# Performance work log

Hardware: AMD Instinct MI355X
Metric: run time of the kernel (lower is better)

Reference implementation:

```python
import jax, jax.numpy as jnp
import numpy as np

DIM_MODEL = 2048
H, DK, DV, L = 16, 128, 128, 2048
LN_EPS = 1e-5


def setup_inputs() -> dict:
    key = jax.random.key(0)
    ks = jax.random.split(key, 8)
    # xavier-ish scale for weights so softmax logits stay sane
    w_scale = (2.0 / (DIM_MODEL + DK)) ** 0.5
    q = jax.random.normal(ks[0], (1, L, DIM_MODEL), dtype=jnp.float32)
    k = jax.random.normal(ks[1], (1, L, DIM_MODEL), dtype=jnp.float32)
    v = jax.random.normal(ks[2], (1, L, DIM_MODEL), dtype=jnp.float32)
    Wq = jax.random.normal(ks[3], (H, DIM_MODEL, DK), dtype=jnp.float32) * w_scale
    Wk = jax.random.normal(ks[4], (H, DIM_MODEL, DK), dtype=jnp.float32) * w_scale
    Wv = jax.random.normal(ks[5], (H, DIM_MODEL, DV), dtype=jnp.float32) * w_scale
    proj_w = jax.random.normal(ks[6], (H * DV, DIM_MODEL), dtype=jnp.float32) * (1.0 / (H * DV) ** 0.5)
    proj_b = jnp.zeros((DIM_MODEL,), dtype=jnp.float32)
    ln_g = jnp.ones((DIM_MODEL,), dtype=jnp.float32)
    ln_b = jnp.zeros((DIM_MODEL,), dtype=jnp.float32)
    return {"q": q, "k": k, "v": v, "Wq": Wq, "Wk": Wk, "Wv": Wv,
            "proj_w": proj_w, "proj_b": proj_b, "ln_g": ln_g, "ln_b": ln_b}


def reference(q, k, v, Wq, Wk, Wv, proj_w, proj_b, ln_g, ln_b):
    # batch must be 1 (enforced by torch.bmm shape rules in the source)
    residual = q  # (1, L, D)
    qs, kv, vv = q[0], k[0], v[0]  # (L, D)
    dim_model = qs.shape[-1]
    temper = jnp.asarray(dim_model, qs.dtype) ** 0.5  # sqrt(dim_model), NOT sqrt(dk)
    qh = jnp.einsum('ld,hdk->hlk', qs, Wq)  # (H, L, dk)
    kh = jnp.einsum('ld,hdk->hlk', kv, Wk)  # (H, L, dk)
    vh = jnp.einsum('ld,hdv->hlv', vv, Wv)  # (H, L, dv)
    scores = jnp.einsum('hqk,hmk->hqm', qh, kh) / temper  # (H, Lq, Lk)
    # faithful quirk: softmax over dim=1 (the QUERY axis)
    attn = jax.nn.softmax(scores, axis=1)
    # attn_dropout / dropout are identity in eval mode
    out = jnp.einsum('hqm,hmv->hqv', attn, vh)  # (H, Lq, dv)
    # cat(split(out, batch=1, dim=0), dim=-1) == move head axis into features
    Lq = out.shape[1]
    out = jnp.transpose(out, (1, 0, 2)).reshape(Lq, -1)  # (Lq, H*dv)
    out = out @ proj_w + proj_b  # (Lq, dim_model)
    y = out[None] + residual  # (1, Lq, D)
    mu = jnp.mean(y, axis=-1, keepdims=True)
    var = jnp.mean((y - mu) ** 2, axis=-1, keepdims=True)
    y = (y - mu) * jax.lax.rsqrt(var + LN_EPS) * ln_g + ln_b
    return (y, attn)
```

## Files before the change

### kernel.cpp

```cpp
#include <hip/hip_runtime.h>
#include <stdint.h>

#define L 2048
#define DMODEL 2048
#define NH 16

typedef __bf16 bf16x8 __attribute__((ext_vector_type(8)));
typedef float f32x4 __attribute__((ext_vector_type(4)));
typedef short s16x4 __attribute__((ext_vector_type(4)));

__device__ __forceinline__ unsigned short f2bf(float f) {
    union { float f; unsigned int i; } w; w.f = f;
    unsigned int u = w.i;
    unsigned int r = u + 0x7fffu + ((u >> 16) & 1u);
    return (unsigned short)(r >> 16);
}

__device__ __forceinline__ void gload_lds16(const unsigned short* g, unsigned short* l) {
    __builtin_amdgcn_global_load_lds(
        (const __attribute__((address_space(1))) void*)g,
        (__attribute__((address_space(3))) void*)l, 16, 0, 0);
}

template<int CMODE, int BM, int BK, int PSM, int SWZ>
__global__ __launch_bounds__(256, 2)
void gemm_bt(const unsigned short* __restrict__ Ag,
             const unsigned short* __restrict__ B,
             void* __restrict__ C,
             int K, int lda, int ldb, int ldc,
             long long sA, long long sB, long long sC, float alpha,
             float* __restrict__ sums)
{
    constexpr int KC8 = BK / 8;
    constexpr int SWM = (KC8 >= 8) ? 7 : (KC8 - 1);
    constexpr int CA  = BM * BK / 2048;
    constexpr int CB  = BK / 16;
    constexpr int MFR = BM / 32;
    constexpr int KG  = BK / 32;

    __shared__ unsigned short As[2][BM * BK];
    __shared__ unsigned short Bs[2][128 * BK];

    int bx, by, bz;
    if constexpr (SWZ == 1) {
        const int xcd = blockIdx.x & 7, rest = blockIdx.x >> 3;
        bx = 0; by = rest & 15; bz = xcd + 8 * (rest >> 4);
    } else if constexpr (SWZ == 2) {
        const int xcd = blockIdx.x & 7, rest = blockIdx.x >> 3;
        const int inner = rest & 255;
        bx = inner & 15; by = inner >> 4; bz = xcd + 8 * (rest >> 8);
    } else if constexpr (SWZ == 3) {
        const int xcd = blockIdx.x & 7, rest = blockIdx.x >> 3;
        bx = xcd + 8 * (rest >> 5); by = rest & 31; bz = 0;
    } else {
        bx = blockIdx.x; by = blockIdx.y; bz = blockIdx.z;
    }

    const int tid  = threadIdx.x;
    const int wave = tid >> 6;
    const int lane = tid & 63;
    const int quad = lane >> 4;
    const int l16  = lane & 15;

    const int tileN = bx * 128;
    const int tileM = by * BM;

    const long long zA = (CMODE == 3) ? (long long)(bz >> 4) : (long long)bz;
    const unsigned short* A16 = Ag + zA * sA;
    B += (long long)bz * sB;

    const int wm = (wave >> 1) * (BM / 2);
    const int wn = (wave & 1) * 64;

    auto stageB = [&](int kk, int buf) {
        #pragma unroll
        for (int j = 0; j < CB; ++j) {
            const int ch = tid + j * 256;
            const int rb = ch / KC8, sl = (ch % KC8) ^ (rb & SWM);
            gload_lds16(B + (long long)(tileN + rb) * ldb + (kk + sl * 8), &Bs[buf][ch * 8]);
        }
    };
    auto stageA = [&](int kk, int buf) {
        #pragma unroll
        for (int j = 0; j < CA; ++j) {
            const int ch = tid + j * 256;
            const int ra = ch / KC8, sl = (ch % KC8) ^ (ra & SWM);
            gload_lds16(A16 + (long long)(tileM + ra) * lda + (kk + sl * 8), &As[buf][ch * 8]);
        }
    };

    f32x4 acc[MFR][4] = {};
    const int nt = K / BK;

    stageA(0, 0);
    stageB(0, 0);
    __syncthreads();

    int cur = 0;
    for (int t = 0; t < nt; ++t) {
        const int nxt = cur ^ 1;
        const int k0n = (t + 1) * BK;
        if (t + 1 < nt) { stageA(k0n, nxt); stageB(k0n, nxt); }

        bf16x8 af[MFR][KG], bfr[4][KG];
        #pragma unroll
        for (int i = 0; i < MFR; ++i) {
            const int rr = wm + i * 16 + l16;
            #pragma unroll
            for (int g = 0; g < KG; ++g)
                af[i][g] = *(const bf16x8*)(&As[cur][rr * BK + ((g * 32 + quad * 8) ^ ((rr & SWM) << 3))]);
        }
        #pragma unroll
        for (int j = 0; j < 4; ++j) {
            const int rr = wn + j * 16 + l16;
            #pragma unroll
            for (int g = 0; g < KG; ++g)
                bfr[j][g] = *(const bf16x8*)(&Bs[cur][rr * BK + ((g * 32 + quad * 8) ^ ((rr & SWM) << 3))]);
        }
        #pragma unroll
        for (int g = 0; g < KG; ++g)
            #pragma unroll
            for (int i = 0; i < MFR; ++i)
                #pragma unroll
                for (int j = 0; j < 4; ++j)
                    acc[i][j] = __builtin_amdgcn_mfma_f32_16x16x32_bf16(af[i][g], bfr[j][g], acc[i][j], 0, 0, 0);

        __syncthreads();
        cur = nxt;
    }

    const long long cb = (long long)bz * sC;
    const float aEff = (CMODE == 3) ? (bz < 16 ? alpha : 1.0f) : alpha;
    if constexpr (CMODE != 4) {
        #pragma unroll
        for (int i = 0; i < MFR; ++i) {
            const int r0 = tileM + wm + i * 16 + quad * 4;
            #pragma unroll
            for (int j = 0; j < 4; ++j) {
                const int c = tileN + wn + j * 16 + l16;
                f32x4 d = acc[i][j];
                if (CMODE == 0) {
                    unsigned short* Cp = (unsigned short*)C + cb;
                    #pragma unroll
                    for (int r = 0; r < 4; ++r)
                        Cp[(long long)(r0 + r) * ldc + c] = f2bf(d[r] * aEff);
                } else if (CMODE == 1) {
                    unsigned short* Cp = (unsigned short*)C + cb + (long long)c * ldc + r0;
                    s16x4 pk;
                    #pragma unroll
                    for (int r = 0; r < 4; ++r) pk[r] = (short)f2bf(d[r] * aEff);
                    *(s16x4*)Cp = pk;
                } else if (CMODE == 2) {
                    float* Cp = (float*)C + cb;
                    #pragma unroll
                    for (int r = 0; r < 4; ++r)
                        Cp[(long long)(r0 + r) * ldc + c] = d[r] * aEff;
                } else {
                    if (bz < 32) {
                        unsigned short* Cp = (unsigned short*)C + cb;
                        #pragma unroll
                        for (int r = 0; r < 4; ++r)
                            Cp[(long long)(r0 + r) * 128 + c] = f2bf(d[r] * aEff);
                    } else {
                        unsigned short* Cp = (unsigned short*)C + cb + (long long)c * 2048 + r0;
                        s16x4 pk;
                        #pragma unroll
                        for (int r = 0; r < 4; ++r) pk[r] = (short)f2bf(d[r]);
                        *(s16x4*)Cp = pk;
                    }
                }
            }
        }
    }

    if constexpr (PSM) {
        float* sc = sums + (long long)bz * 2048;
        #pragma unroll
        for (int j = 0; j < 4; ++j) {
            float ej = 0.f;
            #pragma unroll
            for (int i = 0; i < MFR; ++i)
                #pragma unroll
                for (int r = 0; r < 4; ++r) ej += __expf(acc[i][j][r]);
            ej += __shfl_xor(ej, 16, 64);
            ej += __shfl_xor(ej, 32, 64);
            if (quad == 0)
                atomicAdd(&sc[tileN + wn + j * 16 + l16], ej);
        }
    }
}

__global__ __launch_bounds__(256, 2)
void fused_pv(const unsigned short* __restrict__ qh,
              const unsigned short* __restrict__ kh,
              const unsigned short* __restrict__ vhT,
              const float* __restrict__ sums,
              float* __restrict__ attn, unsigned short* __restrict__ O)
{
    __shared__ unsigned short qh_s[64 * 128];
    __shared__ unsigned short kh_s[2][32 * 128];
    __shared__ unsigned short vh_s[3][128 * 32];
    __shared__ unsigned short p16[2][64 * 32];

    const int tid = threadIdx.x;
    const int wave = tid >> 6, lane = tid & 63, quad = lane >> 4, l16 = lane & 15;
    const int slot = blockIdx.x >> 3;
    const int qt = slot & 31;
    const int h  = (blockIdx.x & 7) + 8 * (slot >> 5);
    const int wA = wave >> 1, wB = wave & 1;
    const unsigned short* qg = qh + (long long)h * 262144 + (long long)qt * 64 * 128;
    const unsigned short* kg = kh + (long long)h * 262144;
    const unsigned short* vg = vhT + (long long)h * 262144;
    const float* smp = sums + h * 2048;
    float* ap = attn + (long long)h * L * L + (long long)qt * 64 * 2048;

    auto stage_kv = [&](int kt, int kb_, int vb_) {
        #pragma unroll
        for (int jj = 0; jj < 2; ++jj) {
            const int c = tid + jj * 256;
            const int rl = c >> 4, sl = (c & 15) ^ (rl & 7);
            gload_lds16(kg + (long long)(kt * 32 + rl) * 128 + sl * 8, &kh_s[kb_][c * 8]);
        }
        #pragma unroll
        for (int jj = 0; jj < 2; ++jj) {
            const int c = tid + jj * 256;
            const int vd = c >> 2, sl = (c & 3) ^ (vd & 3);
            gload_lds16(vg + (long long)vd * 2048 + kt * 32 + sl * 8, &vh_s[vb_][c * 8]);
        }
    };

    #pragma unroll
    for (int jj = 0; jj < 4; ++jj) {
        const int c = tid + jj * 256;
        const int rl = c >> 4, sl = (c & 15) ^ (rl & 7);
        gload_lds16(qg + (long long)rl * 128 + sl * 8, &qh_s[c * 8]);
    }
    stage_kv(0, 0, 0);
    __syncthreads();

    f32x4 acc_o[2][4] = {};
    const int krow = wA * 16 + l16;

    for (int t = 0; t < 64; ++t) {
        const int cb = t & 1;
        const int vb3 = t % 3;
        if (t < 63) stage_kv(t + 1, cb ^ 1, (t + 1) % 3);

        const int kb = t * 32 + wA * 16 + quad * 4;
        const f32x4 sg4 = *(const f32x4*)(smp + kb);

        bf16x8 af[4];
        #pragma unroll
        for (int g = 0; g < 4; ++g)
            af[g] = *(const bf16x8*)(&kh_s[cb][krow * 128 + ((g * 32 + quad * 8) ^ ((krow & 7) << 3))]);
        f32x4 acc_s[2];
        __builtin_amdgcn_s_setprio(1);
        #pragma unroll
        for (int j = 0; j < 2; ++j) {
            const int q = wB * 32 + j * 16 + l16;
            f32x4 s = {};
            #pragma unroll
            for (int g = 0; g < 4; ++g) {
                bf16x8 bq = *(const bf16x8*)(&qh_s[q * 128 + ((g * 32 + quad * 8) ^ ((q & 7) << 3))]);
                s = __builtin_amdgcn_mfma_f32_16x16x32_bf16(af[g], bq, s, 0, 0, 0);
            }
            acc_s[j] = s;
        }
        __builtin_amdgcn_s_setprio(0);

        f32x4 il4;
        #pragma unroll
        for (int r = 0; r < 4; ++r) il4[r] = __builtin_amdgcn_rcpf(sg4[r]);
        #pragma unroll
        for (int j = 0; j < 2; ++j) {
            const int q = wB * 32 + j * 16 + l16;
            f32x4 p;
            #pragma unroll
            for (int r = 0; r < 4; ++r)
                p[r] = __expf(acc_s[j][r]) * il4[r];
            __builtin_nontemporal_store(p, (f32x4*)(ap + (long long)q * 2048 + kb));
            s16x4 pk;
            #pragma unroll
            for (int r = 0; r < 4; ++r) pk[r] = (short)f2bf(p[r]);
            *(s16x4*)(&p16[cb][q * 32 + ((wA * 16 + quad * 4) ^ ((q & 3) << 3))]) = pk;
        }

        __syncthreads();

        bf16x8 pa[2], vb[4];
        #pragma unroll
        for (int i = 0; i < 2; ++i) {
            const int qq = wA * 32 + i * 16 + l16;
            pa[i] = *(const bf16x8*)(&p16[cb][qq * 32 + ((quad * 8) ^ ((qq & 3) << 3))]);
        }
        #pragma unroll
        for (int j = 0; j < 4; ++j) {
            const int vd = wB * 64 + j * 16 + l16;
            vb[j] = *(const bf16x8*)(&vh_s[vb3][vd * 32 + ((quad * 8) ^ ((vd & 3) << 3))]);
        }
        __builtin_amdgcn_s_setprio(1);
        #pragma unroll
        for (int i = 0; i < 2; ++i)
            #pragma unroll
            for (int j = 0; j < 4; ++j)
                acc_o[i][j] = __builtin_amdgcn_mfma_f32_16x16x32_bf16(pa[i], vb[j], acc_o[i][j], 0, 0, 0);
        __builtin_amdgcn_s_setprio(0);
    }

    #pragma unroll
    for (int i = 0; i < 2; ++i) {
        const int q = qt * 64 + wA * 32 + i * 16 + quad * 4;
        #pragma unroll
        for (int j = 0; j < 4; ++j) {
            const int vd = h * 128 + wB * 64 + j * 16 + l16;
            #pragma unroll
            for (int r = 0; r < 4; ++r)
                O[(long long)(q + r) * 2048 + vd] = f2bf(acc_o[i][j][r]);
        }
    }
}

__global__ __launch_bounds__(256)
void cvt_f2b3(const float* __restrict__ a, const float* __restrict__ b,
              const float* __restrict__ c, unsigned short* __restrict__ out)
{
    const float* in = blockIdx.z == 0 ? a : blockIdx.z == 1 ? b : c;
    const long long i = ((long long)blockIdx.x * 256 + threadIdx.x) * 8;
    const float4 f0 = *(const float4*)(in + i);
    const float4 f1 = *(const float4*)(in + i + 4);
    union { int4 v; unsigned short u[8]; } t;
    t.u[0] = f2bf(f0.x); t.u[1] = f2bf(f0.y); t.u[2] = f2bf(f0.z); t.u[3] = f2bf(f0.w);
    t.u[4] = f2bf(f1.x); t.u[5] = f2bf(f1.y); t.u[6] = f2bf(f1.z); t.u[7] = f2bf(f1.w);
    *(int4*)(out + (long long)blockIdx.z * 4194304 + i) = t.v;
}

__global__ __launch_bounds__(256)
void transpose_f2b(const float* __restrict__ in, unsigned short* __restrict__ out,
                   int rows, int cols)
{
    __shared__ float t[32][33];
    const long long base = (long long)blockIdx.z * rows * cols;
    const int c0 = blockIdx.x * 32, r0 = blockIdx.y * 32;
    const int tx = threadIdx.x, ty0 = threadIdx.y;
    #pragma unroll
    for (int jj = 0; jj < 4; ++jj) {
        const int j = ty0 + jj * 8;
        t[j][tx] = in[base + (long long)(r0 + j) * cols + (c0 + tx)];
    }
    __syncthreads();
    #pragma unroll
    for (int jj = 0; jj < 4; ++jj) {
        const int j = ty0 + jj * 8;
        out[base + (long long)(c0 + j) * rows + (r0 + tx)] = f2bf(t[tx][j]);
    }
}

__global__ __launch_bounds__(256)
void transpose_f2b3(const float* __restrict__ Wq, const float* __restrict__ Wk,
                    const float* __restrict__ Wv, unsigned short* __restrict__ out)
{
    __shared__ float t[32][33];
    const int z = blockIdx.z, widx = z >> 4, h = z & 15;
    const float* in = (widx == 0 ? Wq : widx == 1 ? Wk : Wv) + (long long)h * 2048 * 128;
    unsigned short* o = out + (long long)z * 262144;
    const int c0 = blockIdx.x * 32, r0 = blockIdx.y * 32;
    const int tx = threadIdx.x, ty0 = threadIdx.y;
    #pragma unroll
    for (int jj = 0; jj < 4; ++jj) {
        const int j = ty0 + jj * 8;
        t[j][tx] = in[(long long)(r0 + j) * 128 + (c0 + tx)];
    }
    __syncthreads();
    #pragma unroll
    for (int jj = 0; jj < 4; ++jj) {
        const int j = ty0 + jj * 8;
        o[(long long)(c0 + j) * 2048 + (r0 + tx)] = f2bf(t[tx][j]);
    }
}

__global__ __launch_bounds__(256)
void ln_resid(const float* __restrict__ ypre, const float* __restrict__ resid,
              const float* __restrict__ pb, const float* __restrict__ g,
              const float* __restrict__ bta, float* __restrict__ y)
{
    __shared__ float as_[4], as2_[4];
    const int l = blockIdx.x;
    const int tid = threadIdx.x;
    float v[8]; float s = 0.f, s2 = 0.f;
    #pragma unroll
    for (int i = 0; i < 8; ++i) {
        const int d = tid + i * 256;
        float t = ypre[(long long)l * DMODEL + d] + pb[d] + resid[(long long)l * DMODEL + d];
        v[i] = t; s += t; s2 += t * t;
    }
    #pragma unroll
    for (int off = 32; off > 0; off >>= 1) {
        s  += __shfl_down(s, off, 64);
        s2 += __shfl_down(s2, off, 64);
    }
    const int wave = tid >> 6, lane = tid & 63;
    if (lane == 0) { as_[wave] = s; as2_[wave] = s2; }
    __syncthreads();
    const float S  = as_[0] + as_[1] + as_[2] + as_[3];
    const float S2 = as2_[0] + as2_[1] + as2_[2] + as2_[3];
    const float mu  = S * (1.0f / DMODEL);
    const float var = S2 * (1.0f / DMODEL) - mu * mu;
    const float rs  = rsqrtf(var + 1e-5f);
    #pragma unroll
    for (int i = 0; i < 8; ++i) {
        const int d = tid + i * 256;
        y[(long long)l * DMODEL + d] = (v[i] - mu) * rs * g[d] + bta[d];
    }
}

extern "C" void kernel_launch(void* const* d_in, const int* in_sizes, int n_in,
                              void* d_out, int out_size, void* d_ws, size_t ws_size,
                              hipStream_t stream)
{
    const float* q  = (const float*)d_in[0];
    const float* k  = (const float*)d_in[1];
    const float* v  = (const float*)d_in[2];
    const float* Wq = (const float*)d_in[3];
    const float* Wk = (const float*)d_in[4];
    const float* Wv = (const float*)d_in[5];
    const float* Pw = (const float*)d_in[6];
    const float* Pb = (const float*)d_in[7];
    const float* Lg = (const float*)d_in[8];
    const float* Lb = (const float*)d_in[9];

    float* y    = (float*)d_out;
    float* attn = y + (size_t)L * DMODEL;

    const size_t SEG = (size_t)4194304;
    unsigned short* T0  = (unsigned short*)d_ws;
    unsigned short* qh  = T0 + SEG;
    unsigned short* kh  = qh + SEG;
    unsigned short* vhT = kh + SEG;
    unsigned short* O   = vhT + SEG;
    float* ypre  = (float*)qh;
    float* sums  = (float*)d_ws;

    unsigned short* qkvb = (unsigned short*)attn;
    unsigned short* WT   = qkvb + 3 * SEG;

    const float inv_temper = 0.022097086912079608f;
    dim3 tb(32, 8);

    cvt_f2b3<<<dim3(2048, 1, 3), 256, 0, stream>>>(q, k, v, qkvb);
    transpose_f2b3<<<dim3(4, 64, 48), tb, 0, stream>>>(Wq, Wk, Wv, WT);
    hipMemsetAsync(sums, 0, (size_t)NH * 2048 * sizeof(float), stream);

    gemm_bt<3, 128, 64, 0, 1><<<dim3(768), 256, 0, stream>>>(qkvb, WT, qh,
        2048, 2048, 2048, 0, 4194304LL, 262144LL, 262144LL, inv_temper, nullptr);

    gemm_bt<4, 128, 64, 1, 2><<<dim3(4096), 256, 0, stream>>>(qh, kh, nullptr,
        128, 128, 128, 0, 262144LL, 262144LL, 0LL, 1.0f, sums);

    fused_pv<<<dim3(512), 256, 0, stream>>>(qh, kh, vhT, sums, attn, O);

    transpose_f2b<<<dim3(64, 64, 1), tb, 0, stream>>>(Pw, T0, 2048, 2048);
    gemm_bt<2, 64, 64, 0, 3><<<dim3(512), 256, 0, stream>>>(O, T0, (void*)ypre,
        2048, 2048, 2048, 2048, 0LL, 0LL, 0LL, 1.0f, nullptr);

    ln_resid<<<dim3(2048), 256, 0, stream>>>(ypre, q, Pb, Lg, Lb, y);
}
```

Baseline: 577.2 us.

## Merge prep kernels, add dedicated QK stats kernel, keep Q fragments in registers

Three launches (activation bf16 conversion, weight transpose, memset of the softmax sums) become one prep kernel that dispatches on block index. The QK column-sum pass moves from the generic double-buffered gemm to a dedicated kernel that loads the full K=128 tiles into LDS once and writes no output. fused_pv now keeps each wave's Q fragments in registers loaded straight from global memory instead of staging Q through LDS, which frees LDS. This is meant to cut launch overhead and LDS traffic, at the cost of more register pressure and a larger LDS footprint in stats_qk.

```diff
diff --git a/kernel.cpp b/kernel.cpp
--- a/kernel.cpp
+++ b/kernel.cpp
@@ -22,14 +22,13 @@
         (__attribute__((address_space(3))) void*)l, 16, 0, 0);
 }
 
-template<int CMODE, int BM, int BK, int PSM, int SWZ>
+template<int CMODE, int BM, int BK, int SWZ>
 __global__ __launch_bounds__(256, 2)
 void gemm_bt(const unsigned short* __restrict__ Ag,
              const unsigned short* __restrict__ B,
              void* __restrict__ C,
              int K, int lda, int ldb, int ldc,
-             long long sA, long long sB, long long sC, float alpha,
-             float* __restrict__ sums)
+             long long sA, long long sB, long long sC, float alpha)
 {
     constexpr int KC8 = BK / 8;
     constexpr int SWM = (KC8 >= 8) ? 7 : (KC8 - 1);
@@ -45,10 +44,6 @@
     if constexpr (SWZ == 1) {
         const int xcd = blockIdx.x & 7, rest = blockIdx.x >> 3;
         bx = 0; by = rest & 15; bz = xcd + 8 * (rest >> 4);
-    } else if constexpr (SWZ == 2) {
-        const int xcd = blockIdx.x & 7, rest = blockIdx.x >> 3;
-        const int inner = rest & 255;
-        bx = inner & 15; by = inner >> 4; bz = xcd + 8 * (rest >> 8);
     } else if constexpr (SWZ == 3) {
         const int xcd = blockIdx.x & 7, rest = blockIdx.x >> 3;
         bx = xcd + 8 * (rest >> 5); by = rest & 31; bz = 0;
@@ -131,62 +126,110 @@
 
     const long long cb = (long long)bz * sC;
     const float aEff = (CMODE == 3) ? (bz < 16 ? alpha : 1.0f) : alpha;
-    if constexpr (CMODE != 4) {
-        #pragma unroll
-        for (int i = 0; i < MFR; ++i) {
-            const int r0 = tileM + wm + i * 16 + quad * 4;
-            #pragma unroll
-            for (int j = 0; j < 4; ++j) {
-                const int c = tileN + wn + j * 16 + l16;
-                f32x4 d = acc[i][j];
-                if (CMODE == 0) {
+    #pragma unroll
+    for (int i = 0; i < MFR; ++i) {
+        const int r0 = tileM + wm + i * 16 + quad * 4;
+        #pragma unroll
+        for (int j = 0; j < 4; ++j) {
+            const int c = tileN + wn + j * 16 + l16;
+            f32x4 d = acc[i][j];
+            if (CMODE == 0) {
+                unsigned short* Cp = (unsigned short*)C + cb;
+                #pragma unroll
+                for (int r = 0; r < 4; ++r)
+                    Cp[(long long)(r0 + r) * ldc + c] = f2bf(d[r] * aEff);
+            } else if (CMODE == 1) {
+                unsigned short* Cp = (unsigned short*)C + cb + (long long)c * ldc + r0;
+                s16x4 pk;
+                #pragma unroll
+                for (int r = 0; r < 4; ++r) pk[r] = (short)f2bf(d[r] * aEff);
+                *(s16x4*)Cp = pk;
+            } else if (CMODE == 2) {
+                float* Cp = (float*)C + cb;
+                #pragma unroll
+                for (int r = 0; r < 4; ++r)
+                    Cp[(long long)(r0 + r) * ldc + c] = d[r] * aEff;
+            } else {
+                if (bz < 32) {
                     unsigned short* Cp = (unsigned short*)C + cb;
                     #pragma unroll
                     for (int r = 0; r < 4; ++r)
-                        Cp[(long long)(r0 + r) * ldc + c] = f2bf(d[r] * aEff);
-                } else if (CMODE == 1) {
-                    unsigned short* Cp = (unsigned short*)C + cb + (long long)c * ldc + r0;
+                        Cp[(long long)(r0 + r) * 128 + c] = f2bf(d[r] * aEff);
+                } else {
+                    unsigned short* Cp = (unsigned short*)C + cb + (long long)c * 2048 + r0;
                     s16x4 pk;
                     #pragma unroll
-                    for (int r = 0; r < 4; ++r) pk[r] = (short)f2bf(d[r] * aEff);
+                    for (int r = 0; r < 4; ++r) pk[r] = (short)f2bf(d[r]);
                     *(s16x4*)Cp = pk;
-                } else if (CMODE == 2) {
-                    float* Cp = (float*)C + cb;
-                    #pragma unroll
-                    for (int r = 0; r < 4; ++r)
-                        Cp[(long long)(r0 + r) * ldc + c] = d[r] * aEff;
-                } else {
-                    if (bz < 32) {
-                        unsigned short* Cp = (unsigned short*)C + cb;
-                        #pragma unroll
-                        for (int r = 0; r < 4; ++r)
-                            Cp[(long long)(r0 + r) * 128 + c] = f2bf(d[r] * aEff);
-                    } else {
-                        unsigned short* Cp = (unsigned short*)C + cb + (long long)c * 2048 + r0;
-                        s16x4 pk;
-                        #pragma unroll
-                        for (int r = 0; r < 4; ++r) pk[r] = (short)f2bf(d[r]);
-                        *(s16x4*)Cp = pk;
-                    }
                 }
             }
         }
     }
-
-    if constexpr (PSM) {
-        float* sc = sums + (long long)bz * 2048;
+}
+
+__global__ __launch_bounds__(256, 2)
+void stats_qk(const unsigned short* __restrict__ qh,
+              const unsigned short* __restrict__ kh,
+              float* __restrict__ sums)
+{
+    __shared__ unsigned short As[128 * 128];
+    __shared__ unsigned short Bs[128 * 128];
+
+    const int xcd = blockIdx.x & 7, rest = blockIdx.x >> 3;
+    const int inner = rest & 255;
+    const int bx = inner & 15, by = inner >> 4;
+    const int bz = xcd + 8 * (rest >> 8);
+
+    const int tid = threadIdx.x;
+    const int wave = tid >> 6, lane = tid & 63, quad = lane >> 4, l16 = lane & 15;
+    const int tileN = bx * 128, tileM = by * 128;
+    const int wm = (wave >> 1) * 64, wn = (wave & 1) * 64;
+
+    const unsigned short* A16 = qh + (long long)bz * 262144;
+    const unsigned short* B16 = kh + (long long)bz * 262144;
+
+    #pragma unroll
+    for (int j = 0; j < 8; ++j) {
+        const int ch = tid + j * 256;
+        const int rr = ch >> 4, sl = (ch & 15) ^ (rr & 7);
+        gload_lds16(A16 + (long long)(tileM + rr) * 128 + sl * 8, &As[ch * 8]);
+        gload_lds16(B16 + (long long)(tileN + rr) * 128 + sl * 8, &Bs[ch * 8]);
+    }
+    __syncthreads();
+
+    f32x4 acc[4][4] = {};
+    #pragma unroll
+    for (int g = 0; g < 4; ++g) {
+        bf16x8 af[4], bfr[4];
+        #pragma unroll
+        for (int i = 0; i < 4; ++i) {
+            const int rr = wm + i * 16 + l16;
+            af[i] = *(const bf16x8*)(&As[rr * 128 + ((g * 32 + quad * 8) ^ ((rr & 7) << 3))]);
+        }
         #pragma unroll
         for (int j = 0; j < 4; ++j) {
-            float ej = 0.f;
-            #pragma unroll
-            for (int i = 0; i < MFR; ++i)
-                #pragma unroll
-                for (int r = 0; r < 4; ++r) ej += __expf(acc[i][j][r]);
-            ej += __shfl_xor(ej, 16, 64);
-            ej += __shfl_xor(ej, 32, 64);
-            if (quad == 0)
-                atomicAdd(&sc[tileN + wn + j * 16 + l16], ej);
-        }
+            const int rr = wn + j * 16 + l16;
+            bfr[j] = *(const bf16x8*)(&Bs[rr * 128 + ((g * 32 + quad * 8) ^ ((rr & 7) << 3))]);
+        }
+        #pragma unroll
+        for (int i = 0; i < 4; ++i)
+            #pragma unroll
+            for (int j = 0; j < 4; ++j)
+                acc[i][j] = __builtin_amdgcn_mfma_f32_16x16x32_bf16(af[i], bfr[j], acc[i][j], 0, 0, 0);
+    }
+
+    float* sc = sums + (long long)bz * 2048;
+    #pragma unroll
+    for (int j = 0; j < 4; ++j) {
+        float ej = 0.f;
+        #pragma unroll
+        for (int i = 0; i < 4; ++i)
+            #pragma unroll
+            for (int r = 0; r < 4; ++r) ej += __expf(acc[i][j][r]);
+        ej += __shfl_xor(ej, 16, 64);
+        ej += __shfl_xor(ej, 32, 64);
+        if (quad == 0)
+            atomicAdd(&sc[tileN + wn + j * 16 + l16], ej);
     }
 }
 
@@ -197,7 +240,6 @@
               const float* __restrict__ sums,
               float* __restrict__ attn, unsigned short* __restrict__ O)
 {
-    __shared__ unsigned short qh_s[64 * 128];
     __shared__ unsigned short kh_s[2][32 * 128];
     __shared__ unsigned short vh_s[3][128 * 32];
     __shared__ unsigned short p16[2][64 * 32];
@@ -229,11 +271,13 @@
         }
     };
 
-    #pragma unroll
-    for (int jj = 0; jj < 4; ++jj) {
-        const int c = tid + jj * 256;
-        const int rl = c >> 4, sl = (c & 15) ^ (rl & 7);
-        gload_lds16(qg + (long long)rl * 128 + sl * 8, &qh_s[c * 8]);
+    bf16x8 bq[2][4];
+    #pragma unroll
+    for (int j = 0; j < 2; ++j) {
+        const int q = wB * 32 + j * 16 + l16;
+        #pragma unroll
+        for (int g = 0; g < 4; ++g)
+            bq[j][g] = *(const bf16x8*)(qg + (long long)q * 128 + g * 32 + quad * 8);
     }
     stage_kv(0, 0, 0);
     __syncthreads();
@@ -257,13 +301,10 @@
         __builtin_amdgcn_s_setprio(1);
         #pragma unroll
         for (int j = 0; j < 2; ++j) {
-            const int q = wB * 32 + j * 16 + l16;
             f32x4 s = {};
             #pragma unroll
-            for (int g = 0; g < 4; ++g) {
-                bf16x8 bq = *(const bf16x8*)(&qh_s[q * 128 + ((g * 32 + quad * 8) ^ ((q & 7) << 3))]);
-                s = __builtin_amdgcn_mfma_f32_16x16x32_bf16(af[g], bq, s, 0, 0, 0);
-            }
+            for (int g = 0; g < 4; ++g)
+                s = __builtin_amdgcn_mfma_f32_16x16x32_bf16(af[g], bq[j][g], s, 0, 0, 0);
             acc_s[j] = s;
         }
         __builtin_amdgcn_s_setprio(0);
@@ -321,17 +362,52 @@
 }
 
 __global__ __launch_bounds__(256)
-void cvt_f2b3(const float* __restrict__ a, const float* __restrict__ b,
-              const float* __restrict__ c, unsigned short* __restrict__ out)
-{
-    const float* in = blockIdx.z == 0 ? a : blockIdx.z == 1 ? b : c;
-    const long long i = ((long long)blockIdx.x * 256 + threadIdx.x) * 8;
-    const float4 f0 = *(const float4*)(in + i);
-    const float4 f1 = *(const float4*)(in + i + 4);
-    union { int4 v; unsigned short u[8]; } t;
-    t.u[0] = f2bf(f0.x); t.u[1] = f2bf(f0.y); t.u[2] = f2bf(f0.z); t.u[3] = f2bf(f0.w);
-    t.u[4] = f2bf(f1.x); t.u[5] = f2bf(f1.y); t.u[6] = f2bf(f1.z); t.u[7] = f2bf(f1.w);
-    *(int4*)(out + (long long)blockIdx.z * 4194304 + i) = t.v;
+void prep(const float* __restrict__ q, const float* __restrict__ k,
+          const float* __restrict__ v,
+          const float* __restrict__ Wq, const float* __restrict__ Wk,
+          const float* __restrict__ Wv,
+          unsigned short* __restrict__ qkvb, unsigned short* __restrict__ WT,
+          float* __restrict__ sums)
+{
+    __shared__ float t[32][33];
+    const int bid = blockIdx.x;
+    const int tid = threadIdx.x;
+
+    if (bid < 6144) {
+        const int z = bid >> 11, xb = bid & 2047;
+        const float* in = z == 0 ? q : z == 1 ? k : v;
+        const long long i = ((long long)xb * 256 + tid) * 8;
+        const float4 f0 = *(const float4*)(in + i);
+        const float4 f1 = *(const float4*)(in + i + 4);
+        union { int4 v4; unsigned short u[8]; } tt;
+        tt.u[0] = f2bf(f0.x); tt.u[1] = f2bf(f0.y); tt.u[2] = f2bf(f0.z); tt.u[3] = f2bf(f0.w);
+        tt.u[4] = f2bf(f1.x); tt.u[5] = f2bf(f1.y); tt.u[6] = f2bf(f1.z); tt.u[7] = f2bf(f1.w);
+        *(int4*)(qkvb + (long long)z * 4194304 + i) = tt.v4;
+    } else if (bid < 18432) {
+        const int r = bid - 6144;
+        const int z = r >> 8, rr = r & 255;
+        const int bx = rr & 3, by = rr >> 2;
+        const int widx = z >> 4, hh = z & 15;
+        const float* in = (widx == 0 ? Wq : widx == 1 ? Wk : Wv) + (long long)hh * 2048 * 128;
+        unsigned short* o = WT + (long long)z * 262144;
+        const int c0 = bx * 32, r0 = by * 32;
+        const int tx = tid & 31, ty0 = tid >> 5;
+        #pragma unroll
+        for (int jj = 0; jj < 4; ++jj) {
+            const int j = ty0 + jj * 8;
+            t[j][tx] = in[(long long)(r0 + j) * 128 + (c0 + tx)];
+        }
+        __syncthreads();
+        #pragma unroll
+        for (int jj = 0; jj < 4; ++jj) {
+            const int j = ty0 + jj * 8;
+            o[(long long)(c0 + j) * 2048 + (r0 + tx)] = f2bf(t[tx][j]);
+        }
+    } else {
+        const int bt = bid - 18432;
+        float4 zz = {0.f, 0.f, 0.f, 0.f};
+        ((float4*)sums)[bt * 256 + tid] = zz;
+    }
 }
 
 __global__ __launch_bounds__(256)
@@ -352,29 +428,6 @@
     for (int jj = 0; jj < 4; ++jj) {
         const int j = ty0 + jj * 8;
         out[base + (long long)(c0 + j) * rows + (r0 + tx)] = f2bf(t[tx][j]);
-    }
-}
-
-__global__ __launch_bounds__(256)
-void transpose_f2b3(const float* __restrict__ Wq, const float* __restrict__ Wk,
-                    const float* __restrict__ Wv, unsigned short* __restrict__ out)
-{
-    __shared__ float t[32][33];
-    const int z = blockIdx.z, widx = z >> 4, h = z & 15;
-    const float* in = (widx == 0 ? Wq : widx == 1 ? Wk : Wv) + (long long)h * 2048 * 128;
-    unsigned short* o = out + (long long)z * 262144;
-    const int c0 = blockIdx.x * 32, r0 = blockIdx.y * 32;
-    const int tx = threadIdx.x, ty0 = threadIdx.y;
-    #pragma unroll
-    for (int jj = 0; jj < 4; ++jj) {
-        const int j = ty0 + jj * 8;
-        t[j][tx] = in[(long long)(r0 + j) * 128 + (c0 + tx)];
-    }
-    __syncthreads();
-    #pragma unroll
-    for (int jj = 0; jj < 4; ++jj) {
-        const int j = ty0 + jj * 8;
-        o[(long long)(c0 + j) * 2048 + (r0 + tx)] = f2bf(t[tx][j]);
     }
 }
 
@@ -446,21 +499,18 @@
     const float inv_temper = 0.022097086912079608f;
     dim3 tb(32, 8);
 
-    cvt_f2b3<<<dim3(2048, 1, 3), 256, 0, stream>>>(q, k, v, qkvb);
-    transpose_f2b3<<<dim3(4, 64, 48), tb, 0, stream>>>(Wq, Wk, Wv, WT);
-    hipMemsetAsync(sums, 0, (size_t)NH * 2048 * sizeof(float), stream);
-
-    gemm_bt<3, 128, 64, 0, 1><<<dim3(768), 256, 0, stream>>>(qkvb, WT, qh,
-        2048, 2048, 2048, 0, 4194304LL, 262144LL, 262144LL, inv_temper, nullptr);
-
-    gemm_bt<4, 128, 64, 1, 2><<<dim3(4096), 256, 0, stream>>>(qh, kh, nullptr,
-        128, 128, 128, 0, 262144LL, 262144LL, 0LL, 1.0f, sums);
+    prep<<<dim3(18464), 256, 0, stream>>>(q, k, v, Wq, Wk, Wv, qkvb, WT, sums);
+
+    gemm_bt<3, 128, 64, 1><<<dim3(768), 256, 0, stream>>>(qkvb, WT, qh,
+        2048, 2048, 2048, 0, 4194304LL, 262144LL, 262144LL, inv_temper);
+
+    stats_qk<<<dim3(4096), 256, 0, stream>>>(qh, kh, sums);
 
     fused_pv<<<dim3(512), 256, 0, stream>>>(qh, kh, vhT, sums, attn, O);
 
     transpose_f2b<<<dim3(64, 64, 1), tb, 0, stream>>>(Pw, T0, 2048, 2048);
-    gemm_bt<2, 64, 64, 0, 3><<<dim3(512), 256, 0, stream>>>(O, T0, (void*)ypre,
-        2048, 2048, 2048, 2048, 0LL, 0LL, 0LL, 1.0f, nullptr);
+    gemm_bt<2, 64, 64, 3><<<dim3(512), 256, 0, stream>>>(O, T0, (void*)ypre,
+        2048, 2048, 2048, 2048, 0LL, 0LL, 0LL, 1.0f);
 
     ln_resid<<<dim3(2048), 256, 0, stream>>>(ypre, q, Pb, Lg, Lb, y);
 }
```

After: 568.8 us. Within noise of the previous version (-1.4%).
